# Performance work log

Measured on AMD Instinct MI355X. Metric: run time of the kernel, lower is better.

Reference implementation:

```python
import jax, jax.numpy as jnp
from jax import lax
import numpy as np

B, S, E, H, V = 16, 512, 300, 512, 10000


def setup_inputs() -> dict:
    key = jax.random.key(0)
    ks = jax.random.split(key, 7)
    sE = 1.0 / np.sqrt(H)  # torch nn.RNN init scale U(-1/sqrt(H), 1/sqrt(H)); randn*scale is fine for a numeric baseline
    return {
        "x": jax.random.normal(ks[0], (B, S, E), dtype=jnp.float32),
        "W_ih": jax.random.normal(ks[1], (H, E), dtype=jnp.float32) * sE,
        "W_hh": jax.random.normal(ks[2], (H, H), dtype=jnp.float32) * sE,
        "b_ih": jax.random.normal(ks[3], (H,), dtype=jnp.float32) * sE,
        "b_hh": jax.random.normal(ks[4], (H,), dtype=jnp.float32) * sE,
        "W_fc": jax.random.normal(ks[5], (V, H), dtype=jnp.float32) * sE,
        "b_fc": jax.random.normal(ks[6], (V,), dtype=jnp.float32) * sE,
    }


def reference(x, W_ih, W_hh, b_ih, b_hh, W_fc, b_fc):
    # Precompute the input projection for all timesteps: [B,S,H]
    xw = jnp.einsum("bse,he->bsh", x, W_ih) + b_ih + b_hh

    def step(h, xt):
        # h: [B,H], xt: [B,H]
        h = jnp.tanh(xt + h @ W_hh.T)
        return h, h

    h0 = jnp.zeros((x.shape[0], W_hh.shape[0]), dtype=x.dtype)
    _, hs = lax.scan(step, h0, jnp.swapaxes(xw, 0, 1))  # hs: [S,B,H]
    hs = jnp.swapaxes(hs, 0, 1)  # [B,S,H]
    logits = jnp.einsum("bsh,vh->bsv", hs, W_fc) + b_fc  # [B,S,V]
    # Faithful to source: Softmax(dim=1) -> over the SEQUENCE axis
    return jax.nn.softmax(logits, axis=1)
```

## Files before the change

### kernel.cpp

```cpp
#include <hip/hip_runtime.h>
#include <hip/hip_bf16.h>
#include <math.h>

#define B_ 16
#define S_ 512
#define E_ 300
#define H_ 512
#define V_ 10000
#define BS_ (B_ * S_)

#define NSL 16
#define JPB (H_ / NSL)
#define NBLK (B_ * NSL)

typedef __attribute__((ext_vector_type(4))) float f32x4;
typedef __attribute__((ext_vector_type(8))) short bf16x8;
typedef unsigned long long u64;

#define PART_WORDS (4 * B_ * H_)

__global__ __launch_bounds__(256) void k0_init(u64* __restrict__ part) {
  const int idx = blockIdx.x * 256 + threadIdx.x;
  part[idx] = 0xFFFFFFFF00000000ull;
}

__global__ __launch_bounds__(256) void k1_xw(const float* __restrict__ x,
                                             const float* __restrict__ W_ih,
                                             const float* __restrict__ b_ih,
                                             const float* __restrict__ b_hh,
                                             float* __restrict__ xw) {
  __shared__ float As[64][156];
  __shared__ float Ws[64][156];
  const int row0 = blockIdx.x * 64;
  const int col0 = blockIdx.y * 64;
  const int tid = threadIdx.x;
  const int ty = tid >> 4, tx = tid & 15;
  float acc[4][4];
#pragma unroll
  for (int ii = 0; ii < 4; ++ii)
#pragma unroll
    for (int jj = 0; jj < 4; ++jj) acc[ii][jj] = 0.f;

  for (int idx = tid; idx < 64 * 38; idx += 256) {
    const int r = idx / 38, e4 = idx - r * 38;
    *(float4*)&As[r][e4 * 4] =
        *(const float4*)&x[(size_t)(row0 + r) * E_ + e4 * 4];
    *(float4*)&Ws[r][e4 * 4] =
        *(const float4*)&W_ih[(size_t)(col0 + r) * E_ + e4 * 4];
  }
  __syncthreads();
#pragma unroll 2
  for (int e4 = 0; e4 < 38; ++e4) {
    f32x4 a[4], w[4];
#pragma unroll
    for (int ii = 0; ii < 4; ++ii)
      a[ii] = *(const f32x4*)&As[ty + 16 * ii][e4 * 4];
#pragma unroll
    for (int jj = 0; jj < 4; ++jj)
      w[jj] = *(const f32x4*)&Ws[tx + 16 * jj][e4 * 4];
#pragma unroll
    for (int ii = 0; ii < 4; ++ii)
#pragma unroll
      for (int jj = 0; jj < 4; ++jj) {
        const f32x4 p = a[ii] * w[jj];
        acc[ii][jj] += p.x + p.y + p.z + p.w;
      }
  }
  __syncthreads();

  for (int idx = tid; idx < 64 * 37; idx += 256) {
    const int r = idx / 37, e4 = idx - r * 37;
    *(float4*)&As[r][e4 * 4] =
        *(const float4*)&x[(size_t)(row0 + r) * E_ + 152 + e4 * 4];
    *(float4*)&Ws[r][e4 * 4] =
        *(const float4*)&W_ih[(size_t)(col0 + r) * E_ + 152 + e4 * 4];
  }
  __syncthreads();
#pragma unroll 2
  for (int e4 = 0; e4 < 37; ++e4) {
    f32x4 a[4], w[4];
#pragma unroll
    for (int ii = 0; ii < 4; ++ii)
      a[ii] = *(const f32x4*)&As[ty + 16 * ii][e4 * 4];
#pragma unroll
    for (int jj = 0; jj < 4; ++jj)
      w[jj] = *(const f32x4*)&Ws[tx + 16 * jj][e4 * 4];
#pragma unroll
    for (int ii = 0; ii < 4; ++ii)
#pragma unroll
      for (int jj = 0; jj < 4; ++jj) {
        const f32x4 p = a[ii] * w[jj];
        acc[ii][jj] += p.x + p.y + p.z + p.w;
      }
  }

#pragma unroll
  for (int jj = 0; jj < 4; ++jj) {
    const int h = col0 + tx + 16 * jj;
    const float bb = b_ih[h] + b_hh[h];
#pragma unroll
    for (int ii = 0; ii < 4; ++ii)
      xw[(size_t)(row0 + ty + 16 * ii) * H_ + h] = acc[ii][jj] + bb;
  }
}

__device__ __forceinline__ u64 pload(const u64* p) {
  return __hip_atomic_load(p, __ATOMIC_RELAXED, __HIP_MEMORY_SCOPE_AGENT);
}
__device__ __forceinline__ u64 load_sc0(const u64* p) {
  u64 r;
  asm volatile("global_load_dwordx2 %0, %1, off sc0\n\ts_waitcnt vmcnt(0)"
               : "=v"(r) : "v"(p) : "memory");
  return r;
}
__device__ __forceinline__ void store_sc0(u64* p, u64 v) {
  asm volatile("global_store_dwordx2 %0, %1, off sc0" :: "v"(p), "v"(v)
               : "memory");
}

__global__ __launch_bounds__(512) void k2_scan(
    const float* __restrict__ xw, const float* __restrict__ W_hh,
    float* __restrict__ hs, u64* __restrict__ part) {
  const int b = blockIdx.x & 15;
  const int g = blockIdx.x >> 4;
  const int tid = threadIdx.x;
  const int j = tid >> 4;
  const int q = tid & 15;
  const int jg = g * JPB + j;

  __shared__ f32x4 Wp[8 * 512];
  __shared__ f32x4 hp4[2][128];

  {
    const float* wrow = &W_hh[(size_t)jg * H_ + q * 32];
#pragma unroll
    for (int i4 = 0; i4 < 8; ++i4)
      Wp[i4 * 512 + tid] = *(const f32x4*)&wrow[i4 * 4];
  }
  if (tid < 128) hp4[0][tid] = (f32x4)0.f;

  u64* const pf = part + (size_t)b * H_;
  u64* const ps = part + (size_t)(2 * B_ + b) * H_;
  const int kk = ((tid & 63) >> 2) * 32 + (tid >> 6) * 4 + (tid & 3);
  bool fast = true;

  float xwv = xw[(size_t)b * S_ * H_ + jg];
  __syncthreads();

  for (int t = 0; t < S_; ++t) {
    const int cur = t & 1;
    f32x4 a4 = (f32x4)0.f;
#pragma unroll
    for (int i4 = 0; i4 < 8; ++i4) {
      const f32x4 wv = Wp[i4 * 512 + tid];
      const f32x4 hv = hp4[cur][i4 * 16 + q];
      a4 += wv * hv;
    }
    float acc = a4.x + a4.y + a4.z + a4.w;
    acc += __shfl_xor(acc, 1);
    acc += __shfl_xor(acc, 2);
    acc += __shfl_xor(acc, 4);
    acc += __shfl_xor(acc, 8);

    if (q == 0) {
      const float hn = tanhf(xwv + acc);
      const u64 pk =
          ((u64)(unsigned)t << 32) | (u64)(unsigned)__float_as_uint(hn);
      store_sc0(&pf[(size_t)cur * (B_ * H_) + jg], pk);
      __hip_atomic_store(&ps[(size_t)cur * (B_ * H_) + jg], pk,
                         __ATOMIC_RELAXED, __HIP_MEMORY_SCOPE_AGENT);
      hs[((size_t)b * S_ + t) * H_ + jg] = hn;
    }
    const int tn = (t + 1 < S_) ? t + 1 : t;
    const float xw_next = xw[((size_t)b * S_ + tn) * H_ + jg];

    if (t + 1 < S_) {
      u64 v = 0;
      bool got = false;
      const u64* fw = &pf[(size_t)cur * (B_ * H_) + kk];
      if (fast) {
        for (int it = 0; it < 64; ++it) {
          v = load_sc0(fw);
          if ((unsigned)(v >> 32) == (unsigned)t) { got = true; break; }
        }
        if (!got) fast = false;
      }
      if (!got) {
        const u64* sw = &ps[(size_t)cur * (B_ * H_) + kk];
        v = pload(sw);
        while ((unsigned)(v >> 32) != (unsigned)t) v = pload(sw);
      }
      ((float*)&hp4[cur ^ 1][0])[tid] = __uint_as_float((unsigned)v);
    }
    xwv = xw_next;
    __syncthreads();
  }
}

__device__ __forceinline__ unsigned short bf16_rtn(float f) {
  unsigned u = __float_as_uint(f);
  return (unsigned short)((u + 0x7FFFu + ((u >> 16) & 1u)) >> 16);
}
__global__ __launch_bounds__(256) void k5_split(const float* __restrict__ src,
                                                unsigned short* __restrict__ hi,
                                                unsigned short* __restrict__ lo,
                                                int n4) {
  const int i = blockIdx.x * 256 + threadIdx.x;
  if (i >= n4) return;
  const float4 f = *(const float4*)&src[i * 4];
  unsigned short h[4], l[4];
  const float ff[4] = {f.x, f.y, f.z, f.w};
#pragma unroll
  for (int k = 0; k < 4; ++k) {
    h[k] = bf16_rtn(ff[k]);
    const float fh = __uint_as_float((unsigned)h[k] << 16);
    l[k] = bf16_rtn(ff[k] - fh);
  }
  *(ushort4*)&hi[i * 4] = make_ushort4(h[0], h[1], h[2], h[3]);
  *(ushort4*)&lo[i * 4] = make_ushort4(l[0], l[1], l[2], l[3]);
}

__global__ __launch_bounds__(256) void k3_logits(
    const unsigned short* __restrict__ Ahi, const unsigned short* __restrict__ Alo,
    const unsigned short* __restrict__ Bhi, const unsigned short* __restrict__ Blo,
    const float* __restrict__ b_fc, float* __restrict__ out,
    float2* __restrict__ pstats) {
  __shared__ unsigned short Ah[2][128 * 32], Al[2][128 * 32];
  __shared__ unsigned short Bh[2][128 * 32], Bl[2][128 * 32];
  __shared__ float2 sstat[2][2][4][16];
  const int m0 = blockIdx.x * 128;
  const int n0 = blockIdx.y * 128;
  const int tid = threadIdx.x;
  const int lane = tid & 63;
  const int wave = tid >> 6;
  const int wm = wave >> 1, wn = wave & 1;
  const int lr = lane & 15;
  const int lg = lane >> 4;
  const int cxr = (lg ^ (lr & 3)) * 8;

  const unsigned short* gp = (wave == 0) ? Ahi : (wave == 1) ? Alo
                           : (wave == 2) ? Bhi : Blo;
  unsigned short* lp0 = (wave == 0) ? Ah[0] : (wave == 1) ? Al[0]
                      : (wave == 2) ? Bh[0] : Bl[0];
  unsigned short* lp1 = (wave == 0) ? Ah[1] : (wave == 1) ? Al[1]
                      : (wave == 2) ? Bh[1] : Bl[1];
  const bool isB = wave >= 2;
  const int lrow = lane >> 2;
  const int lchunk = (lane & 3) ^ (lrow & 3);

  f32x4 acc[4][4];
#pragma unroll
  for (int mi = 0; mi < 4; ++mi)
#pragma unroll
    for (int ni = 0; ni < 4; ++ni) acc[mi][ni] = (f32x4)0.0f;

  auto STAGE = [&](int k0, unsigned short* dst) {
#pragma unroll
    for (int c16 = 0; c16 < 8; ++c16) {
      const int r = c16 * 16 + lrow;
      const int grow = isB ? min(n0 + r, V_ - 1) : (m0 + r);
      const unsigned short* src = gp + (size_t)grow * H_ + k0 + lchunk * 8;
      __builtin_amdgcn_global_load_lds(
          (const __attribute__((address_space(1))) void*)src,
          (__attribute__((address_space(3))) void*)(dst + c16 * 512), 16, 0, 0);
    }
  };
  auto COMPUTE = [&](int buf) {
    bf16x8 ah[4], al[4], bh[4], bl[4];
#pragma unroll
    for (int i = 0; i < 4; ++i) {
      ah[i] = *(const bf16x8*)&Ah[buf][(wm * 64 + i * 16 + lr) * 32 + cxr];
      al[i] = *(const bf16x8*)&Al[buf][(wm * 64 + i * 16 + lr) * 32 + cxr];
      bh[i] = *(const bf16x8*)&Bh[buf][(wn * 64 + i * 16 + lr) * 32 + cxr];
      bl[i] = *(const bf16x8*)&Bl[buf][(wn * 64 + i * 16 + lr) * 32 + cxr];
    }
#pragma unroll
    for (int mi = 0; mi < 4; ++mi)
#pragma unroll
      for (int ni = 0; ni < 4; ++ni) {
        acc[mi][ni] = __builtin_amdgcn_mfma_f32_16x16x32_bf16(
            ah[mi], bh[ni], acc[mi][ni], 0, 0, 0);
        acc[mi][ni] = __builtin_amdgcn_mfma_f32_16x16x32_bf16(
            ah[mi], bl[ni], acc[mi][ni], 0, 0, 0);
        acc[mi][ni] = __builtin_amdgcn_mfma_f32_16x16x32_bf16(
            al[mi], bh[ni], acc[mi][ni], 0, 0, 0);
      }
  };

  STAGE(0, lp0);
  __syncthreads();
  for (int kt = 0; kt < 16; kt += 2) {
    STAGE((kt + 1) * 32, lp1);
    COMPUTE(0);
    __syncthreads();
    if (kt + 2 < 16) STAGE((kt + 2) * 32, lp0);
    COMPUTE(1);
    __syncthreads();
  }

#pragma unroll
  for (int ni = 0; ni < 4; ++ni) {
    const int v = n0 + wn * 64 + ni * 16 + lr;
    if (v >= V_) continue;
    const float bias = b_fc[v];
#pragma unroll
    for (int mi = 0; mi < 4; ++mi) {
      const int mrow = m0 + wm * 64 + mi * 16 + lg * 4;
#pragma unroll
      for (int r = 0; r < 4; ++r)
        out[(size_t)(mrow + r) * V_ + v] = acc[mi][ni][r] + bias;
    }
  }

  float pm[4], psum[4];
#pragma unroll
  for (int ni = 0; ni < 4; ++ni) {
    const int v = n0 + wn * 64 + ni * 16 + lr;
    float m = -3.4e38f, s = 0.f;
    if (v < V_) {
      const float bias = b_fc[v];
#pragma unroll
      for (int mi = 0; mi < 4; ++mi)
#pragma unroll
        for (int r = 0; r < 4; ++r)
          m = fmaxf(m, acc[mi][ni][r] + bias);
#pragma unroll
      for (int mi = 0; mi < 4; ++mi)
#pragma unroll
        for (int r = 0; r < 4; ++r)
          s += __expf(acc[mi][ni][r] + bias - m);
    }
#pragma unroll
    for (int d = 16; d <= 32; d <<= 1) {
      const float om = __shfl_xor(m, d);
      const float os = __shfl_xor(s, d);
      const float nm = fmaxf(m, om);
      s = s * __expf(m - nm) + os * __expf(om - nm);
      m = nm;
    }
    pm[ni] = m;
    psum[ni] = s;
  }
  __syncthreads();
  if (lg == 0) {
#pragma unroll
    for (int ni = 0; ni < 4; ++ni)
      sstat[wm][wn][ni][lr] = make_float2(pm[ni], psum[ni]);
  }
  __syncthreads();
  if (wm == 0 && lg == 0) {
#pragma unroll
    for (int ni = 0; ni < 4; ++ni) {
      const int v = n0 + wn * 64 + ni * 16 + lr;
      if (v < V_) {
        const float2 s0 = sstat[0][wn][ni][lr];
        const float2 s1 = sstat[1][wn][ni][lr];
        const float nm = fmaxf(s0.x, s1.x);
        const float ss =
            s0.y * __expf(s0.x - nm) + s1.y * __expf(s1.x - nm);
        pstats[(size_t)blockIdx.x * V_ + v] = make_float2(nm, ss);
      }
    }
  }
}

__global__ __launch_bounds__(256) void k4_merge(const float2* __restrict__ pstats,
                                                float* __restrict__ stats) {
  const int gg = blockIdx.x * 256 + threadIdx.x;
  const int b = gg / V_;
  const int v = gg - b * V_;
  float m = -3.4e38f, s = 0.f;
#pragma unroll
  for (int i = 0; i < 4; ++i) {
    const float2 p = pstats[(size_t)(4 * b + i) * V_ + v];
    const float nm = fmaxf(m, p.x);
    s = s * __expf(m - nm) + p.y * __expf(p.x - nm);
    m = nm;
  }
  stats[2 * gg] = m;
  stats[2 * gg + 1] = 1.f / s;
}

__global__ __launch_bounds__(256) void k4_norm(float* __restrict__ logits,
                                               const float* __restrict__ stats) {
  const int bs = blockIdx.y;
  const int b = bs >> 9;
  const int v0 = blockIdx.x * 2048 + threadIdx.x * 8;
  if (v0 >= V_) return;
  float* p = logits + (size_t)bs * V_ + v0;
  const float* st = stats + 2 * (b * V_ + v0);
  const float4 l0 = *(const float4*)&p[0];
  const float4 l1 = *(const float4*)&p[4];
  const float4 s0 = *(const float4*)&st[0];
  const float4 s1 = *(const float4*)&st[4];
  const float4 s2 = *(const float4*)&st[8];
  const float4 s3 = *(const float4*)&st[12];
  float4 o0, o1;
  o0.x = __expf(l0.x - s0.x) * s0.y;
  o0.y = __expf(l0.y - s0.z) * s0.w;
  o0.z = __expf(l0.z - s1.x) * s1.y;
  o0.w = __expf(l0.w - s1.z) * s1.w;
  o1.x = __expf(l1.x - s2.x) * s2.y;
  o1.y = __expf(l1.y - s2.z) * s2.w;
  o1.z = __expf(l1.z - s3.x) * s3.y;
  o1.w = __expf(l1.w - s3.z) * s3.w;
  *(float4*)&p[0] = o0;
  *(float4*)&p[4] = o1;
}

extern "C" void kernel_launch(void* const* d_in, const int* in_sizes, int n_in,
                              void* d_out, int out_size, void* d_ws,
                              size_t ws_size, hipStream_t stream) {
  const float* x    = (const float*)d_in[0];
  const float* W_ih = (const float*)d_in[1];
  const float* W_hh = (const float*)d_in[2];
  const float* b_ih = (const float*)d_in[3];
  const float* b_hh = (const float*)d_in[4];
  const float* W_fc = (const float*)d_in[5];
  const float* b_fc = (const float*)d_in[6];
  float* out = (float*)d_out;

  float* ws = (float*)d_ws;
  float* xw    = ws;
  float* hs    = xw + (size_t)BS_ * H_;
  float* stats = hs + (size_t)BS_ * H_;
  unsigned short* wfc_hi = (unsigned short*)(stats + (size_t)2 * B_ * V_);
  unsigned short* wfc_lo = wfc_hi + (size_t)V_ * H_;
  float2* pstats = (float2*)(wfc_lo + (size_t)V_ * H_);
  u64* part = (u64*)wfc_hi;
  unsigned short* hs_hi = (unsigned short*)xw;
  unsigned short* hs_lo = hs_hi + (size_t)BS_ * H_;

  k0_init<<<PART_WORDS / 256, 256, 0, stream>>>(part);
  k1_xw<<<dim3(BS_ / 64, H_ / 64), 256, 0, stream>>>(x, W_ih, b_ih, b_hh, xw);
  k2_scan<<<NBLK, 512, 0, stream>>>(xw, W_hh, hs, part);
  k5_split<<<((V_ * H_ / 4) + 255) / 256, 256, 0, stream>>>(W_fc, wfc_hi,
                                                            wfc_lo, V_ * H_ / 4);
  k5_split<<<((BS_ * H_ / 4) + 255) / 256, 256, 0, stream>>>(
      hs, hs_hi, hs_lo, BS_ * H_ / 4);
  k3_logits<<<dim3(BS_ / 128, (V_ + 127) / 128), 256, 0, stream>>>(
      hs_hi, hs_lo, wfc_hi, wfc_lo, b_fc, out, pstats);
  k4_merge<<<(B_ * V_) / 256, 256, 0, stream>>>(pstats, stats);
  k4_norm<<<dim3((V_ + 2047) / 2048, BS_), 256, 0, stream>>>(out, stats);
}
```

Baseline: 1.306 ms.

## Offload slow-path publish and hs stores to a dedicated ninth wavefront in RNN scan

```diff
diff --git a/kernel.cpp b/kernel.cpp
--- a/kernel.cpp
+++ b/kernel.cpp
@@ -117,21 +117,27 @@
   asm volatile("global_store_dwordx2 %0, %1, off sc0" :: "v"(p), "v"(v)
                : "memory");
 }
-
-__global__ __launch_bounds__(512) void k2_scan(
+__device__ __forceinline__ void lgkm_barrier() {
+  asm volatile("s_waitcnt lgkmcnt(0)\n\ts_barrier" ::: "memory");
+}
+
+__global__ __launch_bounds__(576) void k2_scan(
     const float* __restrict__ xw, const float* __restrict__ W_hh,
     float* __restrict__ hs, u64* __restrict__ part) {
   const int b = blockIdx.x & 15;
   const int g = blockIdx.x >> 4;
   const int tid = threadIdx.x;
+  const int wid = tid >> 6;
+  const int lane = tid & 63;
   const int j = tid >> 4;
   const int q = tid & 15;
   const int jg = g * JPB + j;
 
   __shared__ f32x4 Wp[8 * 512];
   __shared__ f32x4 hp4[2][128];
-
-  {
+  __shared__ float hname[JPB];
+
+  if (tid < 512) {
     const float* wrow = &W_hh[(size_t)jg * H_ + q * 32];
 #pragma unroll
     for (int i4 = 0; i4 < 8; ++i4)
@@ -144,37 +150,46 @@
   const int kk = ((tid & 63) >> 2) * 32 + (tid >> 6) * 4 + (tid & 3);
   bool fast = true;
 
-  float xwv = xw[(size_t)b * S_ * H_ + jg];
+  float xwv = (tid < 512) ? xw[(size_t)b * S_ * H_ + jg] : 0.f;
   __syncthreads();
 
   for (int t = 0; t < S_; ++t) {
     const int cur = t & 1;
-    f32x4 a4 = (f32x4)0.f;
-#pragma unroll
-    for (int i4 = 0; i4 < 8; ++i4) {
-      const f32x4 wv = Wp[i4 * 512 + tid];
-      const f32x4 hv = hp4[cur][i4 * 16 + q];
-      a4 += wv * hv;
-    }
-    float acc = a4.x + a4.y + a4.z + a4.w;
-    acc += __shfl_xor(acc, 1);
-    acc += __shfl_xor(acc, 2);
-    acc += __shfl_xor(acc, 4);
-    acc += __shfl_xor(acc, 8);
-
-    if (q == 0) {
-      const float hn = tanhf(xwv + acc);
-      const u64 pk =
-          ((u64)(unsigned)t << 32) | (u64)(unsigned)__float_as_uint(hn);
-      store_sc0(&pf[(size_t)cur * (B_ * H_) + jg], pk);
-      __hip_atomic_store(&ps[(size_t)cur * (B_ * H_) + jg], pk,
-                         __ATOMIC_RELAXED, __HIP_MEMORY_SCOPE_AGENT);
-      hs[((size_t)b * S_ + t) * H_ + jg] = hn;
-    }
-    const int tn = (t + 1 < S_) ? t + 1 : t;
-    const float xw_next = xw[((size_t)b * S_ + tn) * H_ + jg];
-
-    if (t + 1 < S_) {
+    if (tid < 512) {
+      f32x4 a4 = (f32x4)0.f;
+#pragma unroll
+      for (int i4 = 0; i4 < 8; ++i4) {
+        const f32x4 wv = Wp[i4 * 512 + tid];
+        const f32x4 hv = hp4[cur][i4 * 16 + q];
+        a4 += wv * hv;
+      }
+      float acc = a4.x + a4.y + a4.z + a4.w;
+      acc += __shfl_xor(acc, 1);
+      acc += __shfl_xor(acc, 2);
+      acc += __shfl_xor(acc, 4);
+      acc += __shfl_xor(acc, 8);
+      if (q == 0) {
+        const float hn = tanhf(xwv + acc);
+        store_sc0(&pf[(size_t)cur * (B_ * H_) + jg],
+                  ((u64)(unsigned)t << 32) | (u64)(unsigned)__float_as_uint(hn));
+        hname[j] = hn;
+        const int tn = (t + 1 < S_) ? t + 1 : t;
+        xwv = xw[((size_t)b * S_ + tn) * H_ + jg];
+      }
+    }
+    lgkm_barrier();
+
+    if (wid == 8) {
+      if (lane < JPB) {
+        const int jp = g * JPB + lane;
+        const float hn = hname[lane];
+        const u64 pk =
+            ((u64)(unsigned)t << 32) | (u64)(unsigned)__float_as_uint(hn);
+        __hip_atomic_store(&ps[(size_t)cur * (B_ * H_) + jp], pk,
+                           __ATOMIC_RELAXED, __HIP_MEMORY_SCOPE_AGENT);
+        hs[((size_t)b * S_ + t) * H_ + jp] = hn;
+      }
+    } else if (t + 1 < S_) {
       u64 v = 0;
       bool got = false;
       const u64* fw = &pf[(size_t)cur * (B_ * H_) + kk];
@@ -192,8 +207,7 @@
       }
       ((float*)&hp4[cur ^ 1][0])[tid] = __uint_as_float((unsigned)v);
     }
-    xwv = xw_next;
-    __syncthreads();
+    lgkm_barrier();
   }
 }
 
@@ -433,7 +447,7 @@
 
   k0_init<<<PART_WORDS / 256, 256, 0, stream>>>(part);
   k1_xw<<<dim3(BS_ / 64, H_ / 64), 256, 0, stream>>>(x, W_ih, b_ih, b_hh, xw);
-  k2_scan<<<NBLK, 512, 0, stream>>>(xw, W_hh, hs, part);
+  k2_scan<<<NBLK, 576, 0, stream>>>(xw, W_hh, hs, part);
   k5_split<<<((V_ * H_ / 4) + 255) / 256, 256, 0, stream>>>(W_fc, wfc_hi,
                                                             wfc_lo, V_ * H_ / 4);
   k5_split<<<((BS_ * H_ / 4) + 255) / 256, 256, 0, stream>>>(
```

Result: no change. 1.289 ms (-1.3%).
